# Performance work log

Hardware: AMD Instinct MI355X
Metric: run time of the kernel (lower is better)

## Reference

```python
import jax, jax.numpy as jnp
import numpy as np

N = 100_000      # nodes
E = 3_200_000    # edges (avg degree 32)
F_IN = 172       # raw node features
HID = 32         # hid_channels
ENC = 8          # encoding_dim
H, C = 2, 16     # heads, per-head channels (TransformerConv 32 -> 2x16)
OUT = 2          # classes
INV_SQRT_C = 1.0 / np.sqrt(C).astype(np.float32)


def setup_inputs() -> dict:
    key = jax.random.key(0)
    ks = jax.random.split(key, 40)
    p = lambda k, shape: (jax.random.normal(k, shape, dtype=jnp.float32) * 0.05)
    return {
        # data tensors
        "x": jax.random.normal(ks[0], (N, F_IN), dtype=jnp.float32),
        "edge_index": jax.random.randint(ks[1], (2, E), 0, N),
        "node_time": jax.random.uniform(ks[2], (N,), dtype=jnp.float32),
        "edge_time": jax.random.uniform(ks[3], (E, 1), dtype=jnp.float32),
        "node_interval": jax.random.uniform(ks[4], (N, 1), dtype=jnp.float32),
        "node_degree": jax.random.uniform(ks[5], (N, 1), dtype=jnp.float32),
        # TimeEncode(32): cos(Linear(1, 32))
        "Wt": p(ks[6], (1, HID)), "bt": p(ks[7], (HID,)),
        # DegreeEncoder / TemporalFrequencyEncoder: Linear(1, 8)
        "Wd": p(ks[8], (1, ENC)), "bd": p(ks[9], (ENC,)),
        "Wtf": p(ks[10], (1, ENC)), "btf": p(ks[11], (ENC,)),
        # w_enc: Linear(8, 8); w_x: Linear(32, 8)
        "Wenc": p(ks[12], (ENC, ENC)), "benc": p(ks[13], (ENC,)),
        "Wx": p(ks[14], (HID, ENC)), "bx": p(ks[15], (ENC,)),
        # lin: Linear(in_channels, 32)
        "Wlin": p(ks[16], (F_IN, HID)), "blin": p(ks[17], (HID,)),
        # lin_combine: Linear(40, 32)
        "Wcomb": p(ks[18], (HID + ENC, HID)), "bcomb": p(ks[19], (HID,)),
        # TransformerConv projections (32 -> heads*16 = 32)
        "Wq": p(ks[20], (HID, H * C)), "bq": p(ks[21], (H * C,)),
        "Wk": p(ks[22], (HID, H * C)), "bk": p(ks[23], (H * C,)),
        "Wv": p(ks[24], (HID, H * C)), "bv": p(ks[25], (H * C,)),
        "We": p(ks[26], (HID, H * C)), "be": p(ks[27], (H * C,)),
        "Wskip": p(ks[28], (HID, H * C)), "bskip": p(ks[29], (H * C,)),
        # out: Linear(32, out_channels)
        "Wout": p(ks[30], (HID, OUT)), "bout": p(ks[31], (OUT,)),
    }


def _segment_softmax(alpha, seg, num_segments):
    # alpha: [E, H], seg: [E] destination indices
    m = jax.ops.segment_max(alpha, seg, num_segments=num_segments)
    a = jnp.exp(alpha - m[seg])
    s = jax.ops.segment_sum(a, seg, num_segments=num_segments)
    return a / (s[seg] + 1e-16)


def reference(x, edge_index, node_time, edge_time, node_interval, node_degree,
              Wt, bt, Wd, bd, Wtf, btf, Wenc, benc, Wx, bx, Wlin, blin,
              Wcomb, bcomb, Wq, bq, Wk, bk, Wv, bv, We, be, Wskip, bskip,
              Wout, bout):
    src, dst = edge_index[0], edge_index[1]
    n = x.shape[0]

    # ---- time encoding of relative edge time: cos(Linear(rel_t)) ----
    rel_t = node_time[src][:, None] - edge_time               # [E, 1]
    rel_t_enc = jnp.cos(rel_t @ Wt + bt)                      # [E, 32]

    # ---- node encoders + attention-gated combine ----
    h1 = x @ Wlin + blin                                      # [N, 32]
    tf_enc = node_interval @ Wtf + btf                        # [N, 8]
    deg_enc = node_degree @ Wd + bd                           # [N, 8]
    encodings = jnp.stack((tf_enc, deg_enc), axis=1)          # [N, 2, 8]
    enc_proj = jnp.tanh(encodings @ Wenc + benc)              # [N, 2, 8]
    x_proj = jnp.tanh(h1 @ Wx + bx)                           # [N, 8]
    score = jnp.einsum('nke,ne->nk', enc_proj, x_proj)        # [N, 2]
    score = jax.nn.softmax(score, axis=1)
    context = jnp.einsum('nke,nk->ne', encodings, score)      # [N, 8]
    h1 = jnp.concatenate((h1, context), axis=1) @ Wcomb + bcomb  # [N, 32]

    # ---- TransformerConv (heads=2, out=16, concat) with edge features ----
    q = (h1 @ Wq + bq).reshape(n, H, C)
    k = (h1 @ Wk + bk).reshape(n, H, C)
    v = (h1 @ Wv + bv).reshape(n, H, C)
    e = (rel_t_enc @ We + be).reshape(-1, H, C)               # [E, H, C]

    k_e = k[src] + e                                          # [E, H, C]
    alpha = jnp.einsum('ehc,ehc->eh', q[dst], k_e) * INV_SQRT_C
    alpha = _segment_softmax(alpha, dst, n)                   # [E, H]
    msg = (v[src] + e) * alpha[..., None]                     # [E, H, C]
    agg = jax.ops.segment_sum(msg, dst, num_segments=n)       # [N, H, C]
    h2 = agg.reshape(n, H * C) + (h1 @ Wskip + bskip)         # root_weight skip

    out = h2 @ Wout + bout                                    # [N, 2]
    return jax.nn.log_softmax(out, axis=1)
```

## Files before the change

### kernel.cpp

```cpp
#include <hip/hip_runtime.h>
#include <hip/hip_bf16.h>
#include <cstdint>


#define FIN 172
#define INV_SQRT_C 0.25f

typedef _Float16 f16x8 __attribute__((ext_vector_type(8)));
typedef float f32x4 __attribute__((ext_vector_type(4)));
typedef short s16x2 __attribute__((ext_vector_type(2)));

__device__ __forceinline__ uint32_t cvt_pk_bf16(float lo, float hi) {
    uint32_t r;
    asm("v_cvt_pk_bf16_f32 %0, %1, %2" : "=v"(r) : "v"(lo), "v"(hi));
    return r;
}
__device__ __forceinline__ float bflo(uint32_t u) {
    union { uint32_t i; float f; } x; x.i = u << 16; return x.f;
}
__device__ __forceinline__ float bfhi(uint32_t u) {
    union { uint32_t i; float f; } x; x.i = u & 0xFFFF0000u; return x.f;
}

__device__ __forceinline__ void pk_atomic_add_bf16(void* addr, uint32_t data) {
#if __has_builtin(__builtin_amdgcn_global_atomic_fadd_v2bf16)
    typedef __attribute__((address_space(1))) s16x2* gp1;
    union { uint32_t u; s16x2 v; } c; c.u = data;
    __builtin_amdgcn_global_atomic_fadd_v2bf16((gp1)(uintptr_t)addr, c.v);
#else
    asm volatile("global_atomic_pk_add_bf16 %0, %1, off"
                 :: "v"((uint64_t)(uintptr_t)addr), "v"(data));
#endif
}

__global__ __launch_bounds__(256) void k1_lin(
    const float* __restrict__ x, const float* __restrict__ Wlin,
    const float* __restrict__ blin, float* __restrict__ h1pre, int n)
{
    const int lane = threadIdx.x & 63;
    const int g = lane >> 4, m = lane & 15;

    f16x8 Bf[6][2];
    #pragma unroll
    for (int s = 0; s < 6; ++s) {
        #pragma unroll
        for (int i = 0; i < 8; ++i) {
            const int k = s * 32 + g * 8 + i;
            Bf[s][0][i] = (_Float16)((k < FIN) ? Wlin[k * 32 + m] : 0.f);
            Bf[s][1][i] = (_Float16)((k < FIN) ? Wlin[k * 32 + 16 + m] : 0.f);
        }
    }
    const float b0 = blin[m], b1 = blin[16 + m];

    const int wid = blockIdx.x * 4 + (threadIdx.x >> 6);
    const int nW  = gridDim.x * 4;
    const int nChunks = (n + 15) / 16;

    for (int c = wid; c < nChunks; c += nW) {
        const int row = c * 16 + m;
        const bool rv = row < n;
        const float* xr = x + (size_t)row * FIN;

        f32x4 acc0 = {0.f, 0.f, 0.f, 0.f};
        f32x4 acc1 = {0.f, 0.f, 0.f, 0.f};
        #pragma unroll
        for (int s = 0; s < 6; ++s) {
            f16x8 A;
            #pragma unroll
            for (int i = 0; i < 8; ++i) {
                const int k = s * 32 + g * 8 + i;
                A[i] = (_Float16)((rv && k < FIN) ? xr[k] : 0.f);
            }
            acc0 = __builtin_amdgcn_mfma_f32_16x16x32_f16(A, Bf[s][0], acc0, 0, 0, 0);
            acc1 = __builtin_amdgcn_mfma_f32_16x16x32_f16(A, Bf[s][1], acc1, 0, 0, 0);
        }
        #pragma unroll
        for (int r = 0; r < 4; ++r) {
            const int node = c * 16 + 4 * g + r;
            if (node < n) {
                h1pre[(size_t)node * 32 + m]      = acc0[r] + b0;
                h1pre[(size_t)node * 32 + 16 + m] = acc1[r] + b1;
            }
        }
    }
}

template <int K, int O>
__device__ __forceinline__ void matvecKO(const float* __restrict__ v,
                                         const float* __restrict__ W,
                                         const float* __restrict__ B,
                                         float* __restrict__ out)
{
    #pragma unroll
    for (int o4 = 0; o4 < O / 4; ++o4) {
        float a0 = B[o4 * 4 + 0], a1 = B[o4 * 4 + 1];
        float a2 = B[o4 * 4 + 2], a3 = B[o4 * 4 + 3];
        #pragma unroll
        for (int k = 0; k < K; ++k) {
            float4 wv = *reinterpret_cast<const float4*>(&W[k * O + o4 * 4]);
            float hv = v[k];
            a0 = fmaf(hv, wv.x, a0);
            a1 = fmaf(hv, wv.y, a1);
            a2 = fmaf(hv, wv.z, a2);
            a3 = fmaf(hv, wv.w, a3);
        }
        out[o4 * 4 + 0] = a0; out[o4 * 4 + 1] = a1;
        out[o4 * 4 + 2] = a2; out[o4 * 4 + 3] = a3;
    }
}

__global__ __launch_bounds__(256) void k2_enc(
    const float* __restrict__ h1pre,
    const float* __restrict__ node_interval, const float* __restrict__ node_degree,
    const float* __restrict__ Wtf, const float* __restrict__ btf,
    const float* __restrict__ Wd,  const float* __restrict__ bd,
    const float* __restrict__ Wenc, const float* __restrict__ benc,
    const float* __restrict__ Wx,  const float* __restrict__ bx,
    const float* __restrict__ Wcomb, const float* __restrict__ bcomb,
    const float* __restrict__ Wq,  const float* __restrict__ bq,
    const float* __restrict__ Wk,  const float* __restrict__ bk,
    const float* __restrict__ Wv,  const float* __restrict__ bv,
    const float* __restrict__ Wskip, const float* __restrict__ bskip,
    uint32_t* __restrict__ q32, uint32_t* __restrict__ kv32,
    float* __restrict__ skipb, int n)
{
    __shared__ __align__(16) float sWenc[64], sWx[256];
    __shared__ float sWtf[8], sbtf[8], sWd[8], sbd[8], sbenc[8], sbx[8];
    __shared__ __align__(16) _Float16 v40s[256][72];
    __shared__ __align__(16) _Float16 h1s[256][40];

    const int t = threadIdx.x;
    if (t < 8) {
        sWtf[t] = Wtf[t]; sbtf[t] = btf[t];
        sWd[t]  = Wd[t];  sbd[t]  = bd[t];
        sbenc[t] = benc[t]; sbx[t] = bx[t];
    }
    if (t < 64) sWenc[t] = Wenc[t];
    if (t < 256) sWx[t] = Wx[t];

    const int nid = blockIdx.x * 256 + t;
    const bool active = nid < n;

    __syncthreads();

    if (active) {
        float h1p[32];
        const float2* hp = reinterpret_cast<const float2*>(h1pre + (size_t)nid * 32);
        #pragma unroll
        for (int i = 0; i < 16; ++i) {
            float2 v2 = hp[i];
            h1p[2 * i] = v2.x; h1p[2 * i + 1] = v2.y;
        }
        const float ti = node_interval[nid], dg = node_degree[nid];
        float tf[8], de[8];
        #pragma unroll
        for (int j = 0; j < 8; ++j) {
            tf[j] = fmaf(ti, sWtf[j], sbtf[j]);
            de[j] = fmaf(dg, sWd[j], sbd[j]);
        }
        float xp[8];
        matvecKO<32, 8>(h1p, sWx, sbx, xp);
        #pragma unroll
        for (int o = 0; o < 8; ++o) xp[o] = tanhf(xp[o]);

        float ep0[8], ep1[8];
        matvecKO<8, 8>(tf, sWenc, sbenc, ep0);
        matvecKO<8, 8>(de, sWenc, sbenc, ep1);
        float sc0 = 0.f, sc1 = 0.f;
        #pragma unroll
        for (int o = 0; o < 8; ++o) {
            sc0 = fmaf(tanhf(ep0[o]), xp[o], sc0);
            sc1 = fmaf(tanhf(ep1[o]), xp[o], sc1);
        }
        const float mm = fmaxf(sc0, sc1);
        const float e0 = __expf(sc0 - mm), e1 = __expf(sc1 - mm);
        const float inv = 1.f / (e0 + e1);
        const float s0 = e0 * inv, s1 = e1 * inv;

        #pragma unroll
        for (int i = 0; i < 32; ++i) v40s[t][i] = (_Float16)h1p[i];
        #pragma unroll
        for (int j = 0; j < 8; ++j)
            v40s[t][32 + j] = (_Float16)fmaf(s0, tf[j], s1 * de[j]);
    } else {
        #pragma unroll
        for (int i = 0; i < 40; ++i) v40s[t][i] = (_Float16)0.f;
    }
    #pragma unroll
    for (int i = 40; i < 64; ++i) v40s[t][i] = (_Float16)0.f;

    __syncthreads();

    const int lane = t & 63;
    const int g = lane >> 4, m = lane & 15;
    const int wv = t >> 6;
    const int node0 = blockIdx.x * 256;

    f16x8 Bc0[2], Bc1[2];
    #pragma unroll
    for (int s = 0; s < 2; ++s)
        #pragma unroll
        for (int i = 0; i < 8; ++i) {
            const int k = s * 32 + g * 8 + i;
            Bc0[s][i] = (_Float16)((k < 40) ? Wcomb[k * 32 + m] : 0.f);
            Bc1[s][i] = (_Float16)((k < 40) ? Wcomb[k * 32 + 16 + m] : 0.f);
        }
    const float bc0 = bcomb[m], bc1 = bcomb[16 + m];

    for (int c = wv; c < 16; c += 4) {
        f32x4 a0 = {0.f, 0.f, 0.f, 0.f};
        f32x4 a1 = {0.f, 0.f, 0.f, 0.f};
        #pragma unroll
        for (int s = 0; s < 2; ++s) {
            const f16x8 A = *reinterpret_cast<const f16x8*>(&v40s[c * 16 + m][s * 32 + g * 8]);
            a0 = __builtin_amdgcn_mfma_f32_16x16x32_f16(A, Bc0[s], a0, 0, 0, 0);
            a1 = __builtin_amdgcn_mfma_f32_16x16x32_f16(A, Bc1[s], a1, 0, 0, 0);
        }
        #pragma unroll
        for (int r = 0; r < 4; ++r) {
            const int nb = c * 16 + 4 * g + r;
            h1s[nb][m]      = (_Float16)(a0[r] + bc0);
            h1s[nb][16 + m] = (_Float16)(a1[r] + bc1);
        }
    }
    __syncthreads();

    f16x8 Bq0, Bq1, Bk0, Bk1, Bv0, Bv1, Bs0, Bs1;
    #pragma unroll
    for (int i = 0; i < 8; ++i) {
        const int k = g * 8 + i;
        Bq0[i] = (_Float16)Wq[k * 32 + m];     Bq1[i] = (_Float16)Wq[k * 32 + 16 + m];
        Bk0[i] = (_Float16)Wk[k * 32 + m];     Bk1[i] = (_Float16)Wk[k * 32 + 16 + m];
        Bv0[i] = (_Float16)Wv[k * 32 + m];     Bv1[i] = (_Float16)Wv[k * 32 + 16 + m];
        Bs0[i] = (_Float16)Wskip[k * 32 + m];  Bs1[i] = (_Float16)Wskip[k * 32 + 16 + m];
    }
    const float bq0 = bq[m], bq1 = bq[16 + m];
    const float bk0 = bk[m], bk1 = bk[16 + m];
    const float bv0 = bv[m], bv1 = bv[16 + m];
    const float bs0 = bskip[m], bs1 = bskip[16 + m];

    for (int c = wv; c < 16; c += 4) {
        const f16x8 A = *reinterpret_cast<const f16x8*>(&h1s[c * 16 + m][g * 8]);

        f32x4 aq0 = {0.f,0.f,0.f,0.f}, aq1 = {0.f,0.f,0.f,0.f};
        f32x4 ak0 = {0.f,0.f,0.f,0.f}, ak1 = {0.f,0.f,0.f,0.f};
        f32x4 av0 = {0.f,0.f,0.f,0.f}, av1 = {0.f,0.f,0.f,0.f};
        f32x4 as0 = {0.f,0.f,0.f,0.f}, as1 = {0.f,0.f,0.f,0.f};
        aq0 = __builtin_amdgcn_mfma_f32_16x16x32_f16(A, Bq0, aq0, 0, 0, 0);
        aq1 = __builtin_amdgcn_mfma_f32_16x16x32_f16(A, Bq1, aq1, 0, 0, 0);
        ak0 = __builtin_amdgcn_mfma_f32_16x16x32_f16(A, Bk0, ak0, 0, 0, 0);
        ak1 = __builtin_amdgcn_mfma_f32_16x16x32_f16(A, Bk1, ak1, 0, 0, 0);
        av0 = __builtin_amdgcn_mfma_f32_16x16x32_f16(A, Bv0, av0, 0, 0, 0);
        av1 = __builtin_amdgcn_mfma_f32_16x16x32_f16(A, Bv1, av1, 0, 0, 0);
        as0 = __builtin_amdgcn_mfma_f32_16x16x32_f16(A, Bs0, as0, 0, 0, 0);
        as1 = __builtin_amdgcn_mfma_f32_16x16x32_f16(A, Bs1, as1, 0, 0, 0);

        #pragma unroll
        for (int r = 0; r < 4; ++r) {
            const int node = node0 + c * 16 + 4 * g + r;
            if (node < n) {
                q32[(size_t)node * 16 + m] =
                    cvt_pk_bf16(aq0[r] + bq0, aq1[r] + bq1);
                uint2 kvd;
                kvd.x = cvt_pk_bf16(ak0[r] + bk0, ak1[r] + bk1);
                kvd.y = cvt_pk_bf16(av0[r] + bv0, av1[r] + bv1);
                *reinterpret_cast<uint2*>(kv32 + (size_t)node * 32 + 2 * m) = kvd;
                skipb[(size_t)node * 32 + m]      = as0[r] + bs0;
                skipb[(size_t)node * 32 + 16 + m] = as1[r] + bs1;
            }
        }
    }
}

__global__ __launch_bounds__(256) void k3_edge(
    const int* __restrict__ ei, const float* __restrict__ node_time,
    const float* __restrict__ edge_time,
    const uint32_t* __restrict__ qp, const uint32_t* __restrict__ kvp,
    const float* __restrict__ Wt, const float* __restrict__ bt,
    const float* __restrict__ We, const float* __restrict__ be,
    unsigned short* __restrict__ agg, unsigned short* __restrict__ den,
    int numE, int nTiles)
{
    const int lane = threadIdx.x & 63;
    const int g = lane >> 4;
    const int m = lane & 15;

    float wtr[8], btr[8];
    f16x8 B0, B1;
    #pragma unroll
    for (int i = 0; i < 8; ++i) {
        const int k = g * 8 + i;
        wtr[i] = Wt[k];
        btr[i] = bt[k];
        B0[i] = (_Float16)We[k * 32 + m];
        B1[i] = (_Float16)We[k * 32 + 16 + m];
    }
    const float be0 = be[m], be1 = be[16 + m];

    const int wid = blockIdx.x * (blockDim.x >> 6) + (threadIdx.x >> 6);
    const int nW  = gridDim.x * (blockDim.x >> 6);

    int tile = wid;
    if (tile >= nTiles) return;

    int srcS = 0, dstS = 0; float etS = 0.f;
    {
        const int eA = tile * 16 + m;
        if (eA < numE) { srcS = ei[eA]; dstS = ei[numE + eA]; etS = edge_time[eA]; }
    }
    float ntC = node_time[srcS];
    float etC = etS;
    int dstrC[4]; uint32_t qwC[4]; uint2 kvwC[4];
    #pragma unroll
    for (int r = 0; r < 4; ++r) {
        const int j = g * 4 + r;
        const int s_ = __shfl(srcS, j);
        dstrC[r] = __shfl(dstS, j);
        qwC[r]  = qp[(size_t)dstrC[r] * 16 + m];
        kvwC[r] = *reinterpret_cast<const uint2*>(kvp + (size_t)s_ * 32 + 2 * m);
    }
    int ntile = tile + nW;
    srcS = 0; dstS = 0; etS = 0.f;
    if (ntile < nTiles) {
        const int eA = ntile * 16 + m;
        if (eA < numE) { srcS = ei[eA]; dstS = ei[numE + eA]; etS = edge_time[eA]; }
    }

    while (true) {
        const float rel = ntC - etC;
        f16x8 A;
        #pragma unroll
        for (int i = 0; i < 8; ++i)
            A[i] = (_Float16)__cosf(fmaf(rel, wtr[i], btr[i]));

        f32x4 acc0 = {0.f, 0.f, 0.f, 0.f};
        f32x4 acc1 = {0.f, 0.f, 0.f, 0.f};
        acc0 = __builtin_amdgcn_mfma_f32_16x16x32_f16(A, B0, acc0, 0, 0, 0);
        acc1 = __builtin_amdgcn_mfma_f32_16x16x32_f16(A, B1, acc1, 0, 0, 0);

        const int e0 = tile * 16;
        uint32_t outD[4], denD[4];
        int outDst[4];
        bool outV[4];
        #pragma unroll
        for (int r = 0; r < 4; ++r) {
            outV[r]   = (e0 + g * 4 + r) < numE;
            outDst[r] = dstrC[r];

            const float ef0 = acc0[r] + be0;
            const float ef1 = acc1[r] + be1;
            const uint32_t uq = qwC[r], uk = kvwC[r].x, uv = kvwC[r].y;

            float p0 = bflo(uq) * (bflo(uk) + ef0);
            float p1 = bfhi(uq) * (bfhi(uk) + ef1);
            #pragma unroll
            for (int s = 1; s < 16; s <<= 1) {
                p0 += __shfl_xor(p0, s);
                p1 += __shfl_xor(p1, s);
            }
            const float w0 = __expf(p0 * INV_SQRT_C);
            const float w1 = __expf(p1 * INV_SQRT_C);

            const float t0 = w0 * (bflo(uv) + ef0);
            const float t1 = w1 * (bfhi(uv) + ef1);
            const float x0 = __shfl_xor(t0, 1);
            const float x1 = __shfl_xor(t1, 1);
            outD[r] = (m & 1) ? cvt_pk_bf16(x1, t1) : cvt_pk_bf16(t0, x0);
            denD[r] = cvt_pk_bf16(w0, w1);
        }

        const bool haveN = ntile < nTiles;
        if (haveN) {
            ntC = node_time[srcS];
            etC = etS;
            #pragma unroll
            for (int r = 0; r < 4; ++r) {
                const int j = g * 4 + r;
                const int s_ = __shfl(srcS, j);
                dstrC[r] = __shfl(dstS, j);
                qwC[r]  = qp[(size_t)dstrC[r] * 16 + m];
                kvwC[r] = *reinterpret_cast<const uint2*>(kvp + (size_t)s_ * 32 + 2 * m);
            }
            const int n2 = ntile + nW;
            srcS = 0; dstS = 0; etS = 0.f;
            if (n2 < nTiles) {
                const int eA = n2 * 16 + m;
                if (eA < numE) { srcS = ei[eA]; dstS = ei[numE + eA]; etS = edge_time[eA]; }
            }
        }

        const int choff = (m & 1) ? (15 + m) : m;
        #pragma unroll
        for (int r = 0; r < 4; ++r) {
            if (outV[r]) {
                pk_atomic_add_bf16(agg + (size_t)outDst[r] * 32 + choff, outD[r]);
                if (m == 0)
                    pk_atomic_add_bf16(den + (size_t)outDst[r] * 32, denD[r]);
            }
        }

        if (!haveN) break;
        tile = ntile; ntile += nW;
    }
}

__global__ __launch_bounds__(256) void k4_out(
    const unsigned short* __restrict__ agg, const unsigned short* __restrict__ den,
    const float* __restrict__ skipb,
    const float* __restrict__ Wout, const float* __restrict__ bout,
    float* __restrict__ out, int n)
{
    __shared__ float sW[64];
    __shared__ float sb[2];
    const int t = threadIdx.x;
    if (t < 64) sW[t] = Wout[t];
    if (t < 2) sb[t] = bout[t];
    __syncthreads();

    const int nid = blockIdx.x * 256 + t;
    if (nid >= n) return;

    const uint32_t ud = reinterpret_cast<const uint32_t*>(den)[(size_t)nid * 16];
    const float inv0 = 1.f / (bflo(ud) + 1e-16f);
    const float inv1 = 1.f / (bfhi(ud) + 1e-16f);
    const uint32_t* ag = reinterpret_cast<const uint32_t*>(agg) + (size_t)nid * 16;
    const float*    sk = skipb + (size_t)nid * 32;

    float o0 = sb[0], o1 = sb[1];
    #pragma unroll
    for (int p = 0; p < 16; ++p) {
        const uint32_t u = ag[p];
        const float iv = (p < 8) ? inv0 : inv1;
        const float hLo = fmaf(bflo(u), iv, sk[2 * p]);
        const float hHi = fmaf(bfhi(u), iv, sk[2 * p + 1]);
        o0 = fmaf(hLo, sW[(2 * p) * 2],     o0);
        o1 = fmaf(hLo, sW[(2 * p) * 2 + 1], o1);
        o0 = fmaf(hHi, sW[(2 * p + 1) * 2],     o0);
        o1 = fmaf(hHi, sW[(2 * p + 1) * 2 + 1], o1);
    }
    const float mm = fmaxf(o0, o1);
    const float lse = mm + __logf(__expf(o0 - mm) + __expf(o1 - mm));
    out[(size_t)nid * 2 + 0] = o0 - lse;
    out[(size_t)nid * 2 + 1] = o1 - lse;
}

extern "C" void kernel_launch(void* const* d_in, const int* in_sizes, int n_in,
                              void* d_out, int out_size, void* d_ws, size_t ws_size,
                              hipStream_t stream)
{
    const float* x             = (const float*)d_in[0];
    const int*   ei            = (const int*)  d_in[1];
    const float* node_time     = (const float*)d_in[2];
    const float* edge_time     = (const float*)d_in[3];
    const float* node_interval = (const float*)d_in[4];
    const float* node_degree   = (const float*)d_in[5];
    const float* Wt    = (const float*)d_in[6];  const float* bt    = (const float*)d_in[7];
    const float* Wd    = (const float*)d_in[8];  const float* bd    = (const float*)d_in[9];
    const float* Wtf   = (const float*)d_in[10]; const float* btf   = (const float*)d_in[11];
    const float* Wenc  = (const float*)d_in[12]; const float* benc  = (const float*)d_in[13];
    const float* Wx    = (const float*)d_in[14]; const float* bx    = (const float*)d_in[15];
    const float* Wlin  = (const float*)d_in[16]; const float* blin  = (const float*)d_in[17];
    const float* Wcomb = (const float*)d_in[18]; const float* bcomb = (const float*)d_in[19];
    const float* Wq    = (const float*)d_in[20]; const float* bq    = (const float*)d_in[21];
    const float* Wk    = (const float*)d_in[22]; const float* bk    = (const float*)d_in[23];
    const float* Wv    = (const float*)d_in[24]; const float* bv    = (const float*)d_in[25];
    const float* We    = (const float*)d_in[26]; const float* be    = (const float*)d_in[27];
    const float* Wskip = (const float*)d_in[28]; const float* bskip = (const float*)d_in[29];
    const float* Wout  = (const float*)d_in[30]; const float* bout  = (const float*)d_in[31];

    const int n    = in_sizes[2];
    const int numE = in_sizes[3];

    char* base = (char*)d_ws;
    uint32_t* q32  = (uint32_t*)base; base += (size_t)n * 16 * 4;
    uint32_t* kv32 = (uint32_t*)base; base += (size_t)n * 32 * 4;
    float* skipb = (float*)base; base += (size_t)n * 32 * 4;
    float* h1pre = (float*)base; base += (size_t)n * 32 * 4;
    unsigned short* agg = (unsigned short*)base; base += (size_t)n * 32 * 2;
    unsigned short* den = (unsigned short*)base; base += (size_t)n * 32 * 2;

    hipMemsetAsync(agg, 0, (size_t)n * 128, stream);

    k1_lin<<<512, 256, 0, stream>>>(x, Wlin, blin, h1pre, n);

    k2_enc<<<(n + 255) / 256, 256, 0, stream>>>(
        h1pre, node_interval, node_degree,
        Wtf, btf, Wd, bd, Wenc, benc, Wx, bx, Wcomb, bcomb,
        Wq, bq, Wk, bk, Wv, bv, Wskip, bskip,
        q32, kv32, skipb, n);

    const int nTiles = (numE + 15) / 16;
    k3_edge<<<4096, 256, 0, stream>>>(
        ei, node_time, edge_time, q32, kv32,
        Wt, bt, We, be, agg, den, numE, nTiles);

    k4_out<<<(n + 255) / 256, 256, 0, stream>>>(
        agg, den, skipb, Wout, bout, (float*)d_out, n);
}
```

Measured before the change: 407.5 us.

## Double-buffer edge gathers two tiles ahead in edge kernel

Result: no change. 409.7 us (+0.5%).

```diff
diff --git a/kernel.cpp b/kernel.cpp
--- a/kernel.cpp
+++ b/kernel.cpp
@@ -21,7 +21,6 @@
 __device__ __forceinline__ float bfhi(uint32_t u) {
     union { uint32_t i; float f; } x; x.i = u & 0xFFFF0000u; return x.f;
 }
-
 __device__ __forceinline__ void pk_atomic_add_bf16(void* addr, uint32_t data) {
 #if __has_builtin(__builtin_amdgcn_global_atomic_fadd_v2bf16)
     typedef __attribute__((address_space(1))) s16x2* gp1;
@@ -272,6 +271,106 @@
     }
 }
 
+struct GatherSet {
+    float nt, et;
+    int   e0;
+    int   dstr[4];
+    uint32_t qw[4];
+    uint2 kvw[4];
+};
+
+__device__ __forceinline__ void stage1(
+    const int* __restrict__ ei, const float* __restrict__ edge_time,
+    int numE, int nTiles, int tile, int m,
+    int& src, int& dst, float& et)
+{
+    src = 0; dst = 0; et = 0.f;
+    if (tile < nTiles) {
+        const int eA = tile * 16 + m;
+        if (eA < numE) { src = ei[eA]; dst = ei[numE + eA]; et = edge_time[eA]; }
+    }
+}
+
+__device__ __forceinline__ void issue_gathers(
+    const uint32_t* __restrict__ qp, const uint32_t* __restrict__ kvp,
+    const float* __restrict__ node_time,
+    int g, int m, int numE, int nTiles, int tile,
+    int srcS, int dstS, float etS, GatherSet& G)
+{
+    G.nt = node_time[srcS];
+    G.et = etS;
+    G.e0 = (tile < nTiles) ? tile * 16 : numE;
+    #pragma unroll
+    for (int r = 0; r < 4; ++r) {
+        const int j = g * 4 + r;
+        const int s_ = __shfl(srcS, j);
+        G.dstr[r] = __shfl(dstS, j);
+        G.qw[r]  = qp[(size_t)G.dstr[r] * 16 + m];
+        G.kvw[r] = *reinterpret_cast<const uint2*>(kvp + (size_t)s_ * 32 + 2 * m);
+    }
+}
+
+__device__ __forceinline__ void compute_tile(
+    const GatherSet& G, const float* wtr, const float* btr,
+    const f16x8& B0, const f16x8& B1, float be0, float be1,
+    int g, int m, int numE,
+    uint32_t* outD, uint32_t* denD, int* outDst, bool* outV)
+{
+    const float rel = G.nt - G.et;
+    f16x8 A;
+    #pragma unroll
+    for (int i = 0; i < 8; ++i)
+        A[i] = (_Float16)__cosf(fmaf(rel, wtr[i], btr[i]));
+
+    f32x4 acc0 = {0.f, 0.f, 0.f, 0.f};
+    f32x4 acc1 = {0.f, 0.f, 0.f, 0.f};
+    acc0 = __builtin_amdgcn_mfma_f32_16x16x32_f16(A, B0, acc0, 0, 0, 0);
+    acc1 = __builtin_amdgcn_mfma_f32_16x16x32_f16(A, B1, acc1, 0, 0, 0);
+
+    #pragma unroll
+    for (int r = 0; r < 4; ++r) {
+        outV[r]   = (G.e0 + g * 4 + r) < numE;
+        outDst[r] = G.dstr[r];
+
+        const float ef0 = acc0[r] + be0;
+        const float ef1 = acc1[r] + be1;
+        const uint32_t uq = G.qw[r], uk = G.kvw[r].x, uv = G.kvw[r].y;
+
+        float p0 = bflo(uq) * (bflo(uk) + ef0);
+        float p1 = bfhi(uq) * (bfhi(uk) + ef1);
+        #pragma unroll
+        for (int s = 1; s < 16; s <<= 1) {
+            p0 += __shfl_xor(p0, s);
+            p1 += __shfl_xor(p1, s);
+        }
+        const float w0 = __expf(p0 * INV_SQRT_C);
+        const float w1 = __expf(p1 * INV_SQRT_C);
+
+        const float t0 = w0 * (bflo(uv) + ef0);
+        const float t1 = w1 * (bfhi(uv) + ef1);
+        const float x0 = __shfl_xor(t0, 1);
+        const float x1 = __shfl_xor(t1, 1);
+        outD[r] = (m & 1) ? cvt_pk_bf16(x1, t1) : cvt_pk_bf16(t0, x0);
+        denD[r] = cvt_pk_bf16(w0, w1);
+    }
+}
+
+__device__ __forceinline__ void issue_atomics(
+    unsigned short* __restrict__ agg, unsigned short* __restrict__ den,
+    const uint32_t* outD, const uint32_t* denD,
+    const int* outDst, const bool* outV, int m)
+{
+    const int choff = (m & 1) ? (15 + m) : m;
+    #pragma unroll
+    for (int r = 0; r < 4; ++r) {
+        if (outV[r]) {
+            pk_atomic_add_bf16(agg + (size_t)outDst[r] * 32 + choff, outD[r]);
+            if (m == 0)
+                pk_atomic_add_bf16(den + (size_t)outDst[r] * 32, denD[r]);
+        }
+    }
+}
+
 __global__ __launch_bounds__(256) void k3_edge(
     const int* __restrict__ ei, const float* __restrict__ node_time,
     const float* __restrict__ edge_time,
@@ -303,104 +402,41 @@
     int tile = wid;
     if (tile >= nTiles) return;
 
-    int srcS = 0, dstS = 0; float etS = 0.f;
-    {
-        const int eA = tile * 16 + m;
-        if (eA < numE) { srcS = ei[eA]; dstS = ei[numE + eA]; etS = edge_time[eA]; }
-    }
-    float ntC = node_time[srcS];
-    float etC = etS;
-    int dstrC[4]; uint32_t qwC[4]; uint2 kvwC[4];
-    #pragma unroll
-    for (int r = 0; r < 4; ++r) {
-        const int j = g * 4 + r;
-        const int s_ = __shfl(srcS, j);
-        dstrC[r] = __shfl(dstS, j);
-        qwC[r]  = qp[(size_t)dstrC[r] * 16 + m];
-        kvwC[r] = *reinterpret_cast<const uint2*>(kvp + (size_t)s_ * 32 + 2 * m);
-    }
-    int ntile = tile + nW;
-    srcS = 0; dstS = 0; etS = 0.f;
-    if (ntile < nTiles) {
-        const int eA = ntile * 16 + m;
-        if (eA < numE) { srcS = ei[eA]; dstS = ei[numE + eA]; etS = edge_time[eA]; }
-    }
+    int srcA, dstA; float etA;
+    int srcB, dstB; float etB;
+    GatherSet GA, GB;
+
+    stage1(ei, edge_time, numE, nTiles, tile, m, srcA, dstA, etA);
+    issue_gathers(qp, kvp, node_time, g, m, numE, nTiles, tile, srcA, dstA, etA, GA);
+    stage1(ei, edge_time, numE, nTiles, tile + 2 * nW, m, srcA, dstA, etA);
+
+    stage1(ei, edge_time, numE, nTiles, tile + nW, m, srcB, dstB, etB);
+    issue_gathers(qp, kvp, node_time, g, m, numE, nTiles, tile + nW, srcB, dstB, etB, GB);
+    stage1(ei, edge_time, numE, nTiles, tile + 3 * nW, m, srcB, dstB, etB);
+
+    uint32_t outD[4], denD[4];
+    int outDst[4];
+    bool outV[4];
 
     while (true) {
-        const float rel = ntC - etC;
-        f16x8 A;
-        #pragma unroll
-        for (int i = 0; i < 8; ++i)
-            A[i] = (_Float16)__cosf(fmaf(rel, wtr[i], btr[i]));
-
-        f32x4 acc0 = {0.f, 0.f, 0.f, 0.f};
-        f32x4 acc1 = {0.f, 0.f, 0.f, 0.f};
-        acc0 = __builtin_amdgcn_mfma_f32_16x16x32_f16(A, B0, acc0, 0, 0, 0);
-        acc1 = __builtin_amdgcn_mfma_f32_16x16x32_f16(A, B1, acc1, 0, 0, 0);
-
-        const int e0 = tile * 16;
-        uint32_t outD[4], denD[4];
-        int outDst[4];
-        bool outV[4];
-        #pragma unroll
-        for (int r = 0; r < 4; ++r) {
-            outV[r]   = (e0 + g * 4 + r) < numE;
-            outDst[r] = dstrC[r];
-
-            const float ef0 = acc0[r] + be0;
-            const float ef1 = acc1[r] + be1;
-            const uint32_t uq = qwC[r], uk = kvwC[r].x, uv = kvwC[r].y;
-
-            float p0 = bflo(uq) * (bflo(uk) + ef0);
-            float p1 = bfhi(uq) * (bfhi(uk) + ef1);
-            #pragma unroll
-            for (int s = 1; s < 16; s <<= 1) {
-                p0 += __shfl_xor(p0, s);
-                p1 += __shfl_xor(p1, s);
-            }
-            const float w0 = __expf(p0 * INV_SQRT_C);
-            const float w1 = __expf(p1 * INV_SQRT_C);
-
-            const float t0 = w0 * (bflo(uv) + ef0);
-            const float t1 = w1 * (bfhi(uv) + ef1);
-            const float x0 = __shfl_xor(t0, 1);
-            const float x1 = __shfl_xor(t1, 1);
-            outD[r] = (m & 1) ? cvt_pk_bf16(x1, t1) : cvt_pk_bf16(t0, x0);
-            denD[r] = cvt_pk_bf16(w0, w1);
-        }
-
-        const bool haveN = ntile < nTiles;
-        if (haveN) {
-            ntC = node_time[srcS];
-            etC = etS;
-            #pragma unroll
-            for (int r = 0; r < 4; ++r) {
-                const int j = g * 4 + r;
-                const int s_ = __shfl(srcS, j);
-                dstrC[r] = __shfl(dstS, j);
-                qwC[r]  = qp[(size_t)dstrC[r] * 16 + m];
-                kvwC[r] = *reinterpret_cast<const uint2*>(kvp + (size_t)s_ * 32 + 2 * m);
-            }
-            const int n2 = ntile + nW;
-            srcS = 0; dstS = 0; etS = 0.f;
-            if (n2 < nTiles) {
-                const int eA = n2 * 16 + m;
-                if (eA < numE) { srcS = ei[eA]; dstS = ei[numE + eA]; etS = edge_time[eA]; }
-            }
-        }
-
-        const int choff = (m & 1) ? (15 + m) : m;
-        #pragma unroll
-        for (int r = 0; r < 4; ++r) {
-            if (outV[r]) {
-                pk_atomic_add_bf16(agg + (size_t)outDst[r] * 32 + choff, outD[r]);
-                if (m == 0)
-                    pk_atomic_add_bf16(den + (size_t)outDst[r] * 32, denD[r]);
-            }
-        }
-
-        if (!haveN) break;
-        tile = ntile; ntile += nW;
+        compute_tile(GA, wtr, btr, B0, B1, be0, be1, g, m, numE,
+                     outD, denD, outDst, outV);
+        issue_gathers(qp, kvp, node_time, g, m, numE, nTiles, tile + 2 * nW,
+                      srcA, dstA, etA, GA);
+        stage1(ei, edge_time, numE, nTiles, tile + 4 * nW, m, srcA, dstA, etA);
+        issue_atomics(agg, den, outD, denD, outDst, outV, m);
+
+        if (tile + nW >= nTiles) break;
+
+        compute_tile(GB, wtr, btr, B0, B1, be0, be1, g, m, numE,
+                     outD, denD, outDst, outV);
+        issue_gathers(qp, kvp, node_time, g, m, numE, nTiles, tile + 3 * nW,
+                      srcB, dstB, etB, GB);
+        stage1(ei, edge_time, numE, nTiles, tile + 5 * nW, m, srcB, dstB, etB);
+        issue_atomics(agg, den, outD, denD, outDst, outV, m);
+
+        tile += 2 * nW;
+        if (tile >= nTiles) break;
     }
 }
 
```
